# Kernel optimization log

Hardware: AMD Instinct MI355X
Metric: run time of the kernel (lower is better)

The kernel has to match this reference:

```python
import jax, jax.numpy as jnp
import numpy as np

B, L, D, H, DEPTH = 64, 384, 128, 8, 6
DH = D // H          # 16
VOCAB = 32000
C_OUT = 128
FF = 4 * D           # reformer_pytorch default ff_mult=4
SELF_VAL = -5e4      # TOKEN_SELF_ATTN_VALUE
MASK_VAL = -1e9      # causal mask value


def layer_norm(x, g, b, eps=1e-5):
    mu = jnp.mean(x, -1, keepdims=True)
    var = jnp.mean((x - mu) ** 2, -1, keepdims=True)
    return (x - mu) * jax.lax.rsqrt(var + eps) * g + b


def attn_block(x, p):
    # PreNorm + LSHSelfAttention in full-QK-attention fallback (seq <= full_attn_thres)
    h = layer_norm(x, p['ln1_g'], p['ln1_b'])
    qk = (h @ p['Wqk']).reshape(B, L, H, DH).transpose(0, 2, 1, 3)  # [B,H,L,DH]
    v = (h @ p['Wv']).reshape(B, L, H, DH).transpose(0, 2, 1, 3)
    # shared QK: q = qk, k = l2-normalized qk
    k = qk / jnp.maximum(jnp.linalg.norm(qk, axis=-1, keepdims=True), 1e-12)
    dots = jnp.einsum('bhid,bhjd->bhij', qk, k) * (DH ** -0.5)
    i = jnp.arange(L)
    eye = i[:, None] == i[None, :]
    future = i[None, :] > i[:, None]
    dots = jnp.where(eye, SELF_VAL, dots)   # token cannot (easily) attend to itself
    dots = jnp.where(future, MASK_VAL, dots)  # causal
    a = jax.nn.softmax(dots, axis=-1)
    o = jnp.einsum('bhij,bhjd->bhid', a, v).transpose(0, 2, 1, 3).reshape(B, L, D)
    return o @ p['Wo'] + p['bo']


def ff_block(x, p):
    h = layer_norm(x, p['ln2_g'], p['ln2_b'])
    h = jax.nn.gelu(h @ p['W1'] + p['b1'], approximate=False)
    return h @ p['W2'] + p['b2']


def forward(x_enc, emb, pos1, pos2, ln1_g, ln1_b, Wqk, Wv, Wo, bo,
            ln2_g, ln2_b, W1, b1, W2, b2, lnf_g, lnf_b, Wp, bp):
    # axial positional embedding (summed mode): (25,D) + (25,D) -> (625,D)
    pos = (pos1[:, None, :] + pos2[None, :, :]).reshape(25 * 25, D)[:L]
    x = emb[x_enc] + pos  # [B,L,D]

    layer_params = dict(ln1_g=ln1_g, ln1_b=ln1_b, Wqk=Wqk, Wv=Wv, Wo=Wo, bo=bo,
                        ln2_g=ln2_g, ln2_b=ln2_b, W1=W1, b1=b1, W2=W2, b2=b2)

    def block(carry, p):
        x1, x2 = carry
        y1 = x1 + attn_block(x2, p)
        y2 = x2 + ff_block(y1, p)
        return (y1, y2), None

    # reversible-net math: duplicate stream, run blocks, average the two halves
    (x1, x2), _ = jax.lax.scan(block, (x, x), layer_params)
    x = layer_norm((x1 + x2) * 0.5, lnf_g, lnf_b)
    return x.reshape(B, L * D) @ Wp + bp  # [B, C_OUT]


def setup_inputs() -> dict:
    key = jax.random.key(0)
    ks = jax.random.split(key, 12)
    s = 0.02
    inp = {
        'x_enc': jax.random.randint(ks[0], (B, L), 0, VOCAB, dtype=jnp.int32),
        'emb': jax.random.normal(ks[1], (VOCAB, D), jnp.float32) * s,
        'pos1': jax.random.normal(ks[2], (25, D), jnp.float32) * s,
        'pos2': jax.random.normal(ks[3], (25, D), jnp.float32) * s,
        'ln1_g': jnp.ones((DEPTH, D), jnp.float32),
        'ln1_b': jnp.zeros((DEPTH, D), jnp.float32),
        'Wqk': jax.random.normal(ks[4], (DEPTH, D, D), jnp.float32) * s,
        'Wv': jax.random.normal(ks[5], (DEPTH, D, D), jnp.float32) * s,
        'Wo': jax.random.normal(ks[6], (DEPTH, D, D), jnp.float32) * s,
        'bo': jnp.zeros((DEPTH, D), jnp.float32),
        'ln2_g': jnp.ones((DEPTH, D), jnp.float32),
        'ln2_b': jnp.zeros((DEPTH, D), jnp.float32),
        'W1': jax.random.normal(ks[7], (DEPTH, D, FF), jnp.float32) * s,
        'b1': jnp.zeros((DEPTH, FF), jnp.float32),
        'W2': jax.random.normal(ks[8], (DEPTH, FF, D), jnp.float32) * s,
        'b2': jnp.zeros((DEPTH, D), jnp.float32),
        'lnf_g': jnp.ones((D,), jnp.float32),
        'lnf_b': jnp.zeros((D,), jnp.float32),
        'Wp': jax.random.normal(ks[9], (L * D, C_OUT), jnp.float32) * s,
        'bp': jnp.zeros((C_OUT,), jnp.float32),
    }
    return inp


def reference(x_enc, emb, pos1, pos2, ln1_g, ln1_b, Wqk, Wv, Wo, bo,
              ln2_g, ln2_b, W1, b1, W2, b2, lnf_g, lnf_b, Wp, bp):
    return forward(x_enc, emb, pos1, pos2, ln1_g, ln1_b, Wqk, Wv, Wo, bo,
                   ln2_g, ln2_b, W1, b1, W2, b2, lnf_g, lnf_b, Wp, bp)
```

## Files before the change

kernel.cpp:

```cpp
#include <hip/hip_runtime.h>
#include <hip/hip_bf16.h>
#include <math.h>

#define BB 64
#define LL 384
#define DD 128
#define HH 8
#define DHH 16
#define DEPTH 6
#define FFD 512
#define MROWS (BB*LL)
#define COUT 128
#define KP (LL*DD)
#define KSPLIT 96
#define KCHUNK 512

typedef short bf16x8 __attribute__((ext_vector_type(8)));
typedef float f32x4 __attribute__((ext_vector_type(4)));

__device__ __forceinline__ unsigned short f2bs(float x) {
    __hip_bfloat16 h = __float2bfloat16(x);
    return *reinterpret_cast<unsigned short*>(&h);
}
__device__ __forceinline__ float bs2f(unsigned short u) {
    unsigned int v = ((unsigned int)u) << 16;
    return __uint_as_float(v);
}
__device__ __forceinline__ float gelu_exact(float x) {
    return 0.5f * x * (1.0f + erff(x * 0.70710678118654752f));
}

__global__ __launch_bounds__(256) void embedln_kernel(
    const int* __restrict__ x_enc, const float* __restrict__ emb,
    const float* __restrict__ pos1, const float* __restrict__ pos2,
    const float* __restrict__ g, const float* __restrict__ b,
    float* __restrict__ x1, float* __restrict__ x2,
    __hip_bfloat16* __restrict__ y)
{
    int wave = threadIdx.x >> 6;
    int lane = threadIdx.x & 63;
    int row = blockIdx.x * 4 + wave;
    int l = row % LL;
    int tok = x_enc[row];
    float2 e  = ((const float2*)(emb + (size_t)tok * DD))[lane];
    float2 p1 = ((const float2*)(pos1 + (l / 25) * DD))[lane];
    float2 p2 = ((const float2*)(pos2 + (l % 25) * DD))[lane];
    float2 v = make_float2(e.x + p1.x + p2.x, e.y + p1.y + p2.y);
    ((float2*)(x1 + (size_t)row * DD))[lane] = v;
    ((float2*)(x2 + (size_t)row * DD))[lane] = v;
    float2 gg = ((const float2*)g)[lane];
    float2 bb = ((const float2*)b)[lane];
    float s = v.x + v.y;
    float sq = v.x * v.x + v.y * v.y;
    #pragma unroll
    for (int off = 32; off > 0; off >>= 1) {
        s += __shfl_down(s, off, 64);
        sq += __shfl_down(sq, off, 64);
    }
    s = __shfl(s, 0, 64);
    sq = __shfl(sq, 0, 64);
    float mean = s * (1.0f / DD);
    float var = sq * (1.0f / DD) - mean * mean;
    float rstd = rsqrtf(var + 1e-5f);
    __hip_bfloat16* yp = y + (size_t)row * DD + lane * 2;
    yp[0] = __float2bfloat16((v.x - mean) * rstd * gg.x + bb.x);
    yp[1] = __float2bfloat16((v.y - mean) * rstd * gg.y + bb.y);
}

__device__ __forceinline__ void castT_body(
    const float* __restrict__ s, __hip_bfloat16* __restrict__ d,
    int K, int N, int kb, int nb)
{
    __shared__ float tile[32][33];
    int tx = threadIdx.x & 31, ty = threadIdx.x >> 5;
    #pragma unroll
    for (int r = 0; r < 32; r += 8)
        tile[r + ty][tx] = s[(size_t)(kb + r + ty) * N + nb + tx];
    __syncthreads();
    #pragma unroll
    for (int r = 0; r < 32; r += 8)
        d[(size_t)(nb + r + ty) * K + kb + tx] = __float2bfloat16(tile[tx][r + ty]);
}

__global__ __launch_bounds__(256) void cast_all_kernel(
    const float* __restrict__ Wqk, const float* __restrict__ Wv,
    const float* __restrict__ Wo,  const float* __restrict__ W1,
    const float* __restrict__ W2,
    __hip_bfloat16* __restrict__ dqk, __hip_bfloat16* __restrict__ dv,
    __hip_bfloat16* __restrict__ dwo, __hip_bfloat16* __restrict__ d1,
    __hip_bfloat16* __restrict__ d2)
{
    int z = blockIdx.x;
    if (z < 288) {
        int m = z >> 4, t = z & 15;
        int which = m / 6, dd = m % 6;
        const float* s = (which == 0 ? Wqk : (which == 1 ? Wv : Wo)) + (size_t)dd * 16384;
        __hip_bfloat16* d = (which == 0 ? dqk : (which == 1 ? dv : dwo))
                            + (size_t)dd * (which == 2 ? 16384 : 32768);
        castT_body(s, d, 128, 128, (t >> 2) * 32, (t & 3) * 32);
    } else if (z < 672) {
        int i = z - 288; int dd = i >> 6; int t = i & 63;
        castT_body(W1 + (size_t)dd * 65536, d1 + (size_t)dd * 65536,
                   128, 512, (t >> 4) * 32, (t & 15) * 32);
    } else {
        int i = z - 672; int dd = i >> 6; int t = i & 63;
        castT_body(W2 + (size_t)dd * 65536, d2 + (size_t)dd * 65536,
                   512, 128, (t >> 2) * 32, (t & 3) * 32);
    }
}

__global__ __launch_bounds__(256) void castWp_kernel(
    const float* __restrict__ src, __hip_bfloat16* __restrict__ dst)
{
    castT_body(src, dst, KP, 128, blockIdx.x * 32, blockIdx.y * 32);
}

template<int K, int N>
__global__ __launch_bounds__(256) void gemm_qkv_kernel(
    const __hip_bfloat16* __restrict__ A, const __hip_bfloat16* __restrict__ Bt,
    __hip_bfloat16* __restrict__ Cdst)
{
    __shared__ unsigned short As[64 * 128];
    __shared__ unsigned short Bs[128 * 128];
    int tid = threadIdx.x;
    int l = tid & 63, w = tid >> 6;
    int wr = w >> 1, wc = w & 1;
    int lr = l & 15, q = l >> 4;
    int m0 = blockIdx.y * 64;
    int n0 = blockIdx.x * 128;

    f32x4 acc[2][4];
    #pragma unroll
    for (int mt = 0; mt < 2; ++mt)
        #pragma unroll
        for (int nt = 0; nt < 4; ++nt) acc[mt][nt] = (f32x4){0.f, 0.f, 0.f, 0.f};

    for (int kt = 0; kt < K; kt += 128) {
        if (kt) __syncthreads();
        #pragma unroll
        for (int p = 0; p < 4; ++p) {
            int n = p * 256 + tid;
            int r = n >> 4;
            int c = (n & 15) ^ (r & 7);
            *(uint4*)&As[n * 8] = *(const uint4*)(A + (size_t)(m0 + r) * K + kt + c * 8);
        }
        #pragma unroll
        for (int p = 0; p < 8; ++p) {
            int n = p * 256 + tid;
            int r = n >> 4;
            int c = (n & 15) ^ (r & 7);
            *(uint4*)&Bs[n * 8] = *(const uint4*)(Bt + (size_t)(n0 + r) * K + kt + c * 8);
        }
        __syncthreads();
        #pragma unroll
        for (int kk = 0; kk < 4; ++kk) {
            bf16x8 afr[2], bfr[4];
            #pragma unroll
            for (int mt = 0; mt < 2; ++mt) {
                int rA = wr * 32 + mt * 16 + lr;
                int cc = (kk * 4 + q) ^ (rA & 7);
                afr[mt] = *(const bf16x8*)&As[(rA * 16 + cc) * 8];
            }
            #pragma unroll
            for (int nt = 0; nt < 4; ++nt) {
                int rB = wc * 64 + nt * 16 + lr;
                int cc = (kk * 4 + q) ^ (rB & 7);
                bfr[nt] = *(const bf16x8*)&Bs[(rB * 16 + cc) * 8];
            }
            #pragma unroll
            for (int mt = 0; mt < 2; ++mt)
                #pragma unroll
                for (int nt = 0; nt < 4; ++nt)
                    acc[mt][nt] = __builtin_amdgcn_mfma_f32_16x16x32_bf16(
                        afr[mt], bfr[nt], acc[mt][nt], 0, 0, 0);
        }
    }

    #pragma unroll
    for (int mt = 0; mt < 2; ++mt)
        #pragma unroll
        for (int nt = 0; nt < 4; ++nt) {
            int col = n0 + wc * 64 + nt * 16 + lr;
            #pragma unroll
            for (int r = 0; r < 4; ++r) {
                int row = m0 + wr * 32 + mt * 16 + q * 4 + r;
                Cdst[(size_t)row * N + col] = __float2bfloat16(acc[mt][nt][r]);
            }
        }
}

__global__ __launch_bounds__(256) void attn_kernel(
    const __hip_bfloat16* __restrict__ qkv, __hip_bfloat16* __restrict__ o)
{
    int z  = blockIdx.x >> 9;
    int bh = blockIdx.x & 511;
    int b = bh >> 3, hh = bh & 7;
    const unsigned short* base = (const unsigned short*)qkv + (size_t)b * LL * 256 + hh * DHH;

    __shared__ unsigned short knb[LL + 2][24];
    __shared__ unsigned short vtb[16][LL + 24];
    __shared__ float cq[LL];
    __shared__ unsigned short ptile[4][16][40];

    int t = threadIdx.x;
    for (int r = t; r < LL; r += 256) {
        const unsigned short* qp = base + (size_t)r * 256;
        unsigned short qs[16], vs16[16];
        *(uint4*)&qs[0]  = *(const uint4*)(qp);
        *(uint4*)&qs[8]  = *(const uint4*)(qp + 8);
        *(uint4*)&vs16[0] = *(const uint4*)(qp + 128);
        *(uint4*)&vs16[8] = *(const uint4*)(qp + 136);
        float q[16];
        #pragma unroll
        for (int d = 0; d < 16; ++d) q[d] = bs2f(qs[d]);
        float nrm = 0.f;
        #pragma unroll
        for (int d = 0; d < 16; ++d) nrm = fmaf(q[d], q[d], nrm);
        float qn = sqrtf(nrm);
        float inv = 1.0f / fmaxf(qn, 1e-12f);
        cq[r] = 0.25f * qn;
        unsigned short kb[16];
        #pragma unroll
        for (int d = 0; d < 16; ++d) kb[d] = f2bs(q[d] * inv);
        *(uint4*)&knb[r][0] = *(uint4*)&kb[0];
        *(uint4*)&knb[r][8] = *(uint4*)&kb[8];
        *(uint4*)&knb[r][16] = make_uint4(0u, 0u, 0u, 0u);
        #pragma unroll
        for (int d = 0; d < 16; ++d) vtb[d][r] = vs16[d];
    }
    if (t < 16) {
        #pragma unroll
        for (int c = 0; c < 24; ++c) vtb[t][LL + c] = 0;
    }
    if (t < 2) {
        #pragma unroll
        for (int c = 0; c < 24; ++c) knb[LL + t][c] = 0;
    }

    int w = t >> 6, l = t & 63;
    int lr = l & 15, q4 = l >> 4;
    __syncthreads();

    bf16x8 zfrag = {0, 0, 0, 0, 0, 0, 0, 0};
    bf16x8 onesf;
    #pragma unroll
    for (int i = 0; i < 8; ++i) onesf[i] = (short)0x3F80;

    int slot = 2 * w + z;
    int strips[3] = { slot, 15 - slot, 16 + slot };
    #pragma unroll
    for (int si = 0; si < 3; ++si) {
        int s = strips[si];
        int r0 = s * 16;
        bf16x8 bq = *(const bf16x8*)&knb[r0 + lr][q4 * 8];
        float ccq = cq[r0 + lr];
        int qg = r0 + lr;

        f32x4 oacc = (f32x4){0.f, 0.f, 0.f, 0.f};
        f32x4 lacc = (f32x4){0.f, 0.f, 0.f, 0.f};

        for (int jt = 0; jt <= s; jt += 2) {
            bf16x8 a0 = *(const bf16x8*)&knb[jt * 16 + lr][(q4 & 1) * 8];
            a0 = (q4 < 2) ? a0 : zfrag;
            bf16x8 a1 = *(const bf16x8*)&knb[(jt + 1) * 16 + lr][(q4 & 1) * 8];
            a1 = (q4 < 2) ? a1 : zfrag;
            f32x4 s0 = __builtin_amdgcn_mfma_f32_16x16x32_bf16(
                a0, bq, (f32x4){0.f, 0.f, 0.f, 0.f}, 0, 0, 0);
            f32x4 s1 = __builtin_amdgcn_mfma_f32_16x16x32_bf16(
                a1, bq, (f32x4){0.f, 0.f, 0.f, 0.f}, 0, 0, 0);

            unsigned int pk0[2], pk1[2];
            #pragma unroll
            for (int h = 0; h < 2; ++h) {
                int ja = jt * 16 + q4 * 4 + 2 * h;
                float pa = __expf(fmaf(s0[2 * h],     ccq, -ccq));
                pa = (ja < qg) ? pa : 0.f;
                float pb = __expf(fmaf(s0[2 * h + 1], ccq, -ccq));
                pb = (ja + 1 < qg) ? pb : 0.f;
                pk0[h] = (unsigned int)f2bs(pa) | ((unsigned int)f2bs(pb) << 16);
                float pc = __expf(fmaf(s1[2 * h],     ccq, -ccq));
                pc = (ja + 16 < qg) ? pc : 0.f;
                float pd = __expf(fmaf(s1[2 * h + 1], ccq, -ccq));
                pd = (ja + 17 < qg) ? pd : 0.f;
                pk1[h] = (unsigned int)f2bs(pc) | ((unsigned int)f2bs(pd) << 16);
            }
            *(uint2*)&ptile[w][lr][q4 * 4]      = make_uint2(pk0[0], pk0[1]);
            *(uint2*)&ptile[w][lr][16 + q4 * 4] = make_uint2(pk1[0], pk1[1]);
            asm volatile("s_waitcnt lgkmcnt(0)" ::: "memory");
            bf16x8 pfrag = *(const bf16x8*)&ptile[w][lr][q4 * 8];
            bf16x8 vfrag = *(const bf16x8*)&vtb[lr][jt * 16 + q4 * 8];
            oacc = __builtin_amdgcn_mfma_f32_16x16x32_bf16(pfrag, vfrag, oacc, 0, 0, 0);
            lacc = __builtin_amdgcn_mfma_f32_16x16x32_bf16(pfrag, onesf, lacc, 0, 0, 0);
        }

        if (s == 0 && q4 == 0) {
            lacc[0] = 1.0f;
            oacc[0] = bs2f(vtb[lr][0]);
        }
        unsigned short* ob = (unsigned short*)o + (size_t)(b * LL + r0) * DD + hh * 16 + lr;
        #pragma unroll
        for (int reg = 0; reg < 4; ++reg) {
            float ov = oacc[reg] / lacc[reg];
            ob[(size_t)(q4 * 4 + reg) * DD] = f2bs(ov);
        }
    }
}

__global__ __launch_bounds__(256) void mega_wolf_kernel(
    const __hip_bfloat16* __restrict__ Ao, const __hip_bfloat16* __restrict__ WoTd,
    const float* __restrict__ bod, float* __restrict__ x1,
    const float* __restrict__ lng, const float* __restrict__ lnb,
    const __hip_bfloat16* __restrict__ W1Td, const float* __restrict__ b1d,
    __hip_bfloat16* __restrict__ hff)
{
    __shared__ unsigned short As[64 * 128];
    __shared__ unsigned short Bs[128 * 128];
    __shared__ unsigned short Hs[64 * 128];
    int tid = threadIdx.x;
    int l = tid & 63, w = tid >> 6;
    int wr = w >> 1, wc = w & 1;
    int lr = l & 15, q = l >> 4;
    int m0 = blockIdx.x * 64;

    f32x4 acc[2][4];
    #pragma unroll
    for (int mt = 0; mt < 2; ++mt)
        #pragma unroll
        for (int nt = 0; nt < 4; ++nt) acc[mt][nt] = (f32x4){0.f, 0.f, 0.f, 0.f};

    #pragma unroll
    for (int p = 0; p < 4; ++p) {
        int n = p * 256 + tid;
        int r = n >> 4;
        int c = (n & 15) ^ (r & 7);
        *(uint4*)&As[n * 8] = *(const uint4*)(Ao + (size_t)(m0 + r) * 128 + c * 8);
    }
    #pragma unroll
    for (int p = 0; p < 8; ++p) {
        int n = p * 256 + tid;
        int r = n >> 4;
        int c = (n & 15) ^ (r & 7);
        *(uint4*)&Bs[n * 8] = *(const uint4*)(WoTd + (size_t)r * 128 + c * 8);
    }
    __syncthreads();
    #pragma unroll
    for (int kk = 0; kk < 4; ++kk) {
        bf16x8 afr[2], bfr[4];
        #pragma unroll
        for (int mt = 0; mt < 2; ++mt) {
            int rA = wr * 32 + mt * 16 + lr;
            int cc = (kk * 4 + q) ^ (rA & 7);
            afr[mt] = *(const bf16x8*)&As[(rA * 16 + cc) * 8];
        }
        #pragma unroll
        for (int nt = 0; nt < 4; ++nt) {
            int rB = wc * 64 + nt * 16 + lr;
            int cc = (kk * 4 + q) ^ (rB & 7);
            bfr[nt] = *(const bf16x8*)&Bs[(rB * 16 + cc) * 8];
        }
        #pragma unroll
        for (int mt = 0; mt < 2; ++mt)
            #pragma unroll
            for (int nt = 0; nt < 4; ++nt)
                acc[mt][nt] = __builtin_amdgcn_mfma_f32_16x16x32_bf16(
                    afr[mt], bfr[nt], acc[mt][nt], 0, 0, 0);
    }

    float* fp = (float*)Bs;
    __syncthreads();
    #pragma unroll
    for (int mt = 0; mt < 2; ++mt)
        #pragma unroll
        for (int nt = 0; nt < 4; ++nt) {
            int col = wc * 64 + nt * 16 + lr;
            float bv = bod[col];
            #pragma unroll
            for (int r = 0; r < 4; ++r) {
                int rowL = wr * 32 + mt * 16 + q * 4 + r;
                fp[rowL * 128 + col] = acc[mt][nt][r] + bv
                                       + x1[(size_t)(m0 + rowL) * 128 + col];
            }
        }
    __syncthreads();
    {
        int rl = tid >> 2, sub = tid & 3;
        float s = 0.f, sq = 0.f;
        #pragma unroll
        for (int c4 = 0; c4 < 8; ++c4) {
            float4 v = *(const float4*)&fp[rl * 128 + sub * 32 + c4 * 4];
            s  += (v.x + v.y) + (v.z + v.w);
            sq += (v.x * v.x + v.y * v.y) + (v.z * v.z + v.w * v.w);
        }
        s  += __shfl_xor(s, 1);  s  += __shfl_xor(s, 2);
        sq += __shfl_xor(sq, 1); sq += __shfl_xor(sq, 2);
        float mean = s * (1.0f / 128.0f);
        float var  = sq * (1.0f / 128.0f) - mean * mean;
        float rstd = rsqrtf(var + 1e-5f);
        #pragma unroll
        for (int c4 = 0; c4 < 8; ++c4) {
            int col = sub * 32 + c4 * 4;
            float4 v  = *(const float4*)&fp[rl * 128 + col];
            *(float4*)(x1 + (size_t)(m0 + rl) * 128 + col) = v;
            float4 g4 = *(const float4*)(lng + col);
            float4 b4 = *(const float4*)(lnb + col);
            unsigned short pk[4];
            pk[0] = f2bs((v.x - mean) * rstd * g4.x + b4.x);
            pk[1] = f2bs((v.y - mean) * rstd * g4.y + b4.y);
            pk[2] = f2bs((v.z - mean) * rstd * g4.z + b4.z);
            pk[3] = f2bs((v.w - mean) * rstd * g4.w + b4.w);
            int addr = rl * 128 + (((col >> 3) ^ (rl & 7)) << 3) + (col & 7);
            *(ushort4*)&Hs[addr] = *(ushort4*)&pk[0];
        }
    }
    __syncthreads();

    for (int nc = 0; nc < 4; ++nc) {
        if (nc) __syncthreads();
        #pragma unroll
        for (int p = 0; p < 8; ++p) {
            int n = p * 256 + tid;
            int r = n >> 4;
            int c = (n & 15) ^ (r & 7);
            *(uint4*)&Bs[n * 8] = *(const uint4*)(W1Td + (size_t)(nc * 128 + r) * 128 + c * 8);
        }
        __syncthreads();
        f32x4 a2[2][4];
        #pragma unroll
        for (int mt = 0; mt < 2; ++mt)
            #pragma unroll
            for (int nt = 0; nt < 4; ++nt) a2[mt][nt] = (f32x4){0.f, 0.f, 0.f, 0.f};
        #pragma unroll
        for (int kk = 0; kk < 4; ++kk) {
            bf16x8 afr[2], bfr[4];
            #pragma unroll
            for (int mt = 0; mt < 2; ++mt) {
                int rA = wr * 32 + mt * 16 + lr;
                int cc = (kk * 4 + q) ^ (rA & 7);
                afr[mt] = *(const bf16x8*)&Hs[(rA * 16 + cc) * 8];
            }
            #pragma unroll
            for (int nt = 0; nt < 4; ++nt) {
                int rB = wc * 64 + nt * 16 + lr;
                int cc = (kk * 4 + q) ^ (rB & 7);
                bfr[nt] = *(const bf16x8*)&Bs[(rB * 16 + cc) * 8];
            }
            #pragma unroll
            for (int mt = 0; mt < 2; ++mt)
                #pragma unroll
                for (int nt = 0; nt < 4; ++nt)
                    a2[mt][nt] = __builtin_amdgcn_mfma_f32_16x16x32_bf16(
                        afr[mt], bfr[nt], a2[mt][nt], 0, 0, 0);
        }
        #pragma unroll
        for (int mt = 0; mt < 2; ++mt)
            #pragma unroll
            for (int nt = 0; nt < 4; ++nt) {
                int colg = nc * 128 + wc * 64 + nt * 16 + lr;
                float bv = b1d[colg];
                #pragma unroll
                for (int r = 0; r < 4; ++r) {
                    int row = m0 + wr * 32 + mt * 16 + q * 4 + r;
                    hff[(size_t)row * 512 + colg] =
                        __float2bfloat16(gelu_exact(a2[mt][nt][r] + bv));
                }
            }
    }
}

template<bool LAST>
__global__ __launch_bounds__(256) void mega_ffq_kernel(
    const __hip_bfloat16* __restrict__ Ahff, const __hip_bfloat16* __restrict__ W2Td,
    const float* __restrict__ b2d, float* __restrict__ x2,
    const float* __restrict__ x1,
    const float* __restrict__ lng, const float* __restrict__ lnb,
    const __hip_bfloat16* __restrict__ WqvTd, __hip_bfloat16* __restrict__ qkv,
    __hip_bfloat16* __restrict__ hout)
{
    __shared__ unsigned short As[64 * 128];
    __shared__ unsigned short Bs[128 * 128];
    __shared__ unsigned short Hs[64 * 128];
    int tid = threadIdx.x;
    int l = tid & 63, w = tid >> 6;
    int wr = w >> 1, wc = w & 1;
    int lr = l & 15, q = l >> 4;
    int m0 = blockIdx.x * 64;

    f32x4 acc[2][4];
    #pragma unroll
    for (int mt = 0; mt < 2; ++mt)
        #pragma unroll
        for (int nt = 0; nt < 4; ++nt) acc[mt][nt] = (f32x4){0.f, 0.f, 0.f, 0.f};

    for (int kt = 0; kt < 512; kt += 128) {
        if (kt) __syncthreads();
        #pragma unroll
        for (int p = 0; p < 4; ++p) {
            int n = p * 256 + tid;
            int r = n >> 4;
            int c = (n & 15) ^ (r & 7);
            *(uint4*)&As[n * 8] = *(const uint4*)(Ahff + (size_t)(m0 + r) * 512 + kt + c * 8);
        }
        #pragma unroll
        for (int p = 0; p < 8; ++p) {
            int n = p * 256 + tid;
            int r = n >> 4;
            int c = (n & 15) ^ (r & 7);
            *(uint4*)&Bs[n * 8] = *(const uint4*)(W2Td + (size_t)r * 512 + kt + c * 8);
        }
        __syncthreads();
        #pragma unroll
        for (int kk = 0; kk < 4; ++kk) {
            bf16x8 afr[2], bfr[4];
            #pragma unroll
            for (int mt = 0; mt < 2; ++mt) {
                int rA = wr * 32 + mt * 16 + lr;
                int cc = (kk * 4 + q) ^ (rA & 7);
                afr[mt] = *(const bf16x8*)&As[(rA * 16 + cc) * 8];
            }
            #pragma unroll
            for (int nt = 0; nt < 4; ++nt) {
                int rB = wc * 64 + nt * 16 + lr;
                int cc = (kk * 4 + q) ^ (rB & 7);
                bfr[nt] = *(const bf16x8*)&Bs[(rB * 16 + cc) * 8];
            }
            #pragma unroll
            for (int mt = 0; mt < 2; ++mt)
                #pragma unroll
                for (int nt = 0; nt < 4; ++nt)
                    acc[mt][nt] = __builtin_amdgcn_mfma_f32_16x16x32_bf16(
                        afr[mt], bfr[nt], acc[mt][nt], 0, 0, 0);
        }
    }

    float* fp = (float*)Bs;
    __syncthreads();
    #pragma unroll
    for (int mt = 0; mt < 2; ++mt)
        #pragma unroll
        for (int nt = 0; nt < 4; ++nt) {
            int col = wc * 64 + nt * 16 + lr;
            float bv = b2d[col];
            #pragma unroll
            for (int r = 0; r < 4; ++r) {
                int rowL = wr * 32 + mt * 16 + q * 4 + r;
                fp[rowL * 128 + col] = acc[mt][nt][r] + bv
                                       + x2[(size_t)(m0 + rowL) * 128 + col];
            }
        }
    __syncthreads();
    {
        int rl = tid >> 2, sub = tid & 3;
        float s = 0.f, sq = 0.f;
        #pragma unroll
        for (int c4 = 0; c4 < 8; ++c4) {
            float4 v = *(const float4*)&fp[rl * 128 + sub * 32 + c4 * 4];
            if (LAST) {
                float4 xo = *(const float4*)(x1 + (size_t)(m0 + rl) * 128 + sub * 32 + c4 * 4);
                v.x = (v.x + xo.x) * 0.5f; v.y = (v.y + xo.y) * 0.5f;
                v.z = (v.z + xo.z) * 0.5f; v.w = (v.w + xo.w) * 0.5f;
            }
            s  += (v.x + v.y) + (v.z + v.w);
            sq += (v.x * v.x + v.y * v.y) + (v.z * v.z + v.w * v.w);
        }
        s  += __shfl_xor(s, 1);  s  += __shfl_xor(s, 2);
        sq += __shfl_xor(sq, 1); sq += __shfl_xor(sq, 2);
        float mean = s * (1.0f / 128.0f);
        float var  = sq * (1.0f / 128.0f) - mean * mean;
        float rstd = rsqrtf(var + 1e-5f);
        #pragma unroll
        for (int c4 = 0; c4 < 8; ++c4) {
            int col = sub * 32 + c4 * 4;
            float4 v = *(const float4*)&fp[rl * 128 + col];
            if (LAST) {
                float4 xo = *(const float4*)(x1 + (size_t)(m0 + rl) * 128 + col);
                v.x = (v.x + xo.x) * 0.5f; v.y = (v.y + xo.y) * 0.5f;
                v.z = (v.z + xo.z) * 0.5f; v.w = (v.w + xo.w) * 0.5f;
            } else {
                *(float4*)(x2 + (size_t)(m0 + rl) * 128 + col) = v;
            }
            float4 g4 = *(const float4*)(lng + col);
            float4 b4 = *(const float4*)(lnb + col);
            unsigned short pk[4];
            pk[0] = f2bs((v.x - mean) * rstd * g4.x + b4.x);
            pk[1] = f2bs((v.y - mean) * rstd * g4.y + b4.y);
            pk[2] = f2bs((v.z - mean) * rstd * g4.z + b4.z);
            pk[3] = f2bs((v.w - mean) * rstd * g4.w + b4.w);
            if (LAST) {
                *(ushort4*)((unsigned short*)hout + (size_t)(m0 + rl) * 128 + col)
                    = *(ushort4*)&pk[0];
            } else {
                int addr = rl * 128 + (((col >> 3) ^ (rl & 7)) << 3) + (col & 7);
                *(ushort4*)&Hs[addr] = *(ushort4*)&pk[0];
            }
        }
    }
    __syncthreads();

    if (!LAST) {
        for (int nc = 0; nc < 2; ++nc) {
            if (nc) __syncthreads();
            #pragma unroll
            for (int p = 0; p < 8; ++p) {
                int n = p * 256 + tid;
                int r = n >> 4;
                int c = (n & 15) ^ (r & 7);
                *(uint4*)&Bs[n * 8] = *(const uint4*)(WqvTd + (size_t)(nc * 128 + r) * 128 + c * 8);
            }
            __syncthreads();
            f32x4 a2[2][4];
            #pragma unroll
            for (int mt = 0; mt < 2; ++mt)
                #pragma unroll
                for (int nt = 0; nt < 4; ++nt) a2[mt][nt] = (f32x4){0.f, 0.f, 0.f, 0.f};
            #pragma unroll
            for (int kk = 0; kk < 4; ++kk) {
                bf16x8 afr[2], bfr[4];
                #pragma unroll
                for (int mt = 0; mt < 2; ++mt) {
                    int rA = wr * 32 + mt * 16 + lr;
                    int cc = (kk * 4 + q) ^ (rA & 7);
                    afr[mt] = *(const bf16x8*)&Hs[(rA * 16 + cc) * 8];
                }
                #pragma unroll
                for (int nt = 0; nt < 4; ++nt) {
                    int rB = wc * 64 + nt * 16 + lr;
                    int cc = (kk * 4 + q) ^ (rB & 7);
                    bfr[nt] = *(const bf16x8*)&Bs[(rB * 16 + cc) * 8];
                }
                #pragma unroll
                for (int mt = 0; mt < 2; ++mt)
                    #pragma unroll
                    for (int nt = 0; nt < 4; ++nt)
                        a2[mt][nt] = __builtin_amdgcn_mfma_f32_16x16x32_bf16(
                            afr[mt], bfr[nt], a2[mt][nt], 0, 0, 0);
            }
            #pragma unroll
            for (int mt = 0; mt < 2; ++mt)
                #pragma unroll
                for (int nt = 0; nt < 4; ++nt) {
                    int colg = nc * 128 + wc * 64 + nt * 16 + lr;
                    #pragma unroll
                    for (int r = 0; r < 4; ++r) {
                        int row = m0 + wr * 32 + mt * 16 + q * 4 + r;
                        qkv[(size_t)row * 256 + colg] = __float2bfloat16(a2[mt][nt][r]);
                    }
                }
        }
    }
}

__global__ __launch_bounds__(256) void final_mfma_kernel(
    const __hip_bfloat16* __restrict__ A, const __hip_bfloat16* __restrict__ Bt,
    float* __restrict__ partials)
{
    __shared__ unsigned short As[64 * 128];
    __shared__ unsigned short Bs[128 * 128];
    int tid = threadIdx.x;
    int l = tid & 63, w = tid >> 6;
    int wr = w >> 1, wc = w & 1;
    int lr = l & 15, q = l >> 4;
    int kbase = blockIdx.x * KCHUNK;

    f32x4 acc[2][4];
    #pragma unroll
    for (int mt = 0; mt < 2; ++mt)
        #pragma unroll
        for (int nt = 0; nt < 4; ++nt) acc[mt][nt] = (f32x4){0.f, 0.f, 0.f, 0.f};

    for (int kt = 0; kt < KCHUNK; kt += 128) {
        if (kt) __syncthreads();
        #pragma unroll
        for (int p = 0; p < 4; ++p) {
            int n = p * 256 + tid;
            int r = n >> 4;
            int c = (n & 15) ^ (r & 7);
            *(uint4*)&As[n * 8] = *(const uint4*)(A + (size_t)r * KP + kbase + kt + c * 8);
        }
        #pragma unroll
        for (int p = 0; p < 8; ++p) {
            int n = p * 256 + tid;
            int r = n >> 4;
            int c = (n & 15) ^ (r & 7);
            *(uint4*)&Bs[n * 8] = *(const uint4*)(Bt + (size_t)r * KP + kbase + kt + c * 8);
        }
        __syncthreads();
        #pragma unroll
        for (int kk = 0; kk < 4; ++kk) {
            bf16x8 afr[2], bfr[4];
            #pragma unroll
            for (int mt = 0; mt < 2; ++mt) {
                int rA = wr * 32 + mt * 16 + lr;
                int cc = (kk * 4 + q) ^ (rA & 7);
                afr[mt] = *(const bf16x8*)&As[(rA * 16 + cc) * 8];
            }
            #pragma unroll
            for (int nt = 0; nt < 4; ++nt) {
                int rB = wc * 64 + nt * 16 + lr;
                int cc = (kk * 4 + q) ^ (rB & 7);
                bfr[nt] = *(const bf16x8*)&Bs[(rB * 16 + cc) * 8];
            }
            #pragma unroll
            for (int mt = 0; mt < 2; ++mt)
                #pragma unroll
                for (int nt = 0; nt < 4; ++nt)
                    acc[mt][nt] = __builtin_amdgcn_mfma_f32_16x16x32_bf16(
                        afr[mt], bfr[nt], acc[mt][nt], 0, 0, 0);
        }
    }

    float* dst = partials + (size_t)blockIdx.x * (64 * 128);
    #pragma unroll
    for (int mt = 0; mt < 2; ++mt)
        #pragma unroll
        for (int nt = 0; nt < 4; ++nt) {
            int col = wc * 64 + nt * 16 + lr;
            #pragma unroll
            for (int r = 0; r < 4; ++r) {
                int row = wr * 32 + mt * 16 + q * 4 + r;
                dst[row * 128 + col] = acc[mt][nt][r];
            }
        }
}

__global__ __launch_bounds__(256) void final_reduce_kernel(
    const float* __restrict__ partials, const float* __restrict__ bp,
    float* __restrict__ out)
{
    int j = blockIdx.x * 256 + threadIdx.x;
    float s = bp[j & (COUT - 1)];
    #pragma unroll 8
    for (int p = 0; p < KSPLIT; ++p)
        s += partials[(size_t)p * 8192 + j];
    out[j] = s;
}

extern "C" void kernel_launch(void* const* d_in, const int* in_sizes, int n_in,
                              void* d_out, int out_size, void* d_ws, size_t ws_size,
                              hipStream_t stream)
{
    const int*   x_enc = (const int*)  d_in[0];
    const float* emb   = (const float*)d_in[1];
    const float* pos1  = (const float*)d_in[2];
    const float* pos2  = (const float*)d_in[3];
    const float* ln1_g = (const float*)d_in[4];
    const float* ln1_b = (const float*)d_in[5];
    const float* Wqk   = (const float*)d_in[6];
    const float* Wv    = (const float*)d_in[7];
    const float* Wo    = (const float*)d_in[8];
    const float* bo    = (const float*)d_in[9];
    const float* ln2_g = (const float*)d_in[10];
    const float* ln2_b = (const float*)d_in[11];
    const float* W1    = (const float*)d_in[12];
    const float* b1    = (const float*)d_in[13];
    const float* W2    = (const float*)d_in[14];
    const float* b2    = (const float*)d_in[15];
    const float* lnf_g = (const float*)d_in[16];
    const float* lnf_b = (const float*)d_in[17];
    const float* Wp    = (const float*)d_in[18];
    const float* bp    = (const float*)d_in[19];
    float* out = (float*)d_out;

    const size_t SZ = (size_t)MROWS * DD;
    float* ws_f = (float*)d_ws;
    float* x1 = ws_f;
    float* x2 = ws_f + SZ;
    __hip_bfloat16* hff  = (__hip_bfloat16*)(ws_f + 2 * SZ);
    __hip_bfloat16* h_bf = (__hip_bfloat16*)(ws_f + 4 * SZ);
    __hip_bfloat16* o_bf = h_bf + SZ;
    __hip_bfloat16* wqvT = o_bf + SZ;
    __hip_bfloat16* woT  = wqvT + 6 * 32768;
    __hip_bfloat16* w1T  = woT  + 6 * 16384;
    __hip_bfloat16* w2T  = w1T  + 6 * 65536;
    __hip_bfloat16* WpT  = w2T  + 6 * 65536;
    __hip_bfloat16* qkv  = WpT;
    float* partials = (float*)(WpT + (size_t)COUT * KP);

    cast_all_kernel<<<dim3(1056), dim3(256), 0, stream>>>(
        Wqk, Wv, Wo, W1, W2, wqvT, wqvT + 16384, woT, w1T, w2T);
    embedln_kernel<<<dim3(MROWS / 4), dim3(256), 0, stream>>>(
        x_enc, emb, pos1, pos2, ln1_g, ln1_b, x1, x2, h_bf);
    gemm_qkv_kernel<128, 256><<<dim3(2, MROWS / 64), dim3(256), 0, stream>>>(
        h_bf, wqvT, qkv);

    for (int d = 0; d < DEPTH; ++d) {
        attn_kernel<<<dim3(BB * HH * 2), dim3(256), 0, stream>>>(qkv, o_bf);
        mega_wolf_kernel<<<dim3(MROWS / 64), dim3(256), 0, stream>>>(
            o_bf, woT + (size_t)d * 16384, bo + d * DD, x1,
            ln2_g + d * DD, ln2_b + d * DD,
            w1T + (size_t)d * 65536, b1 + d * FFD, hff);
        if (d < DEPTH - 1) {
            mega_ffq_kernel<false><<<dim3(MROWS / 64), dim3(256), 0, stream>>>(
                hff, w2T + (size_t)d * 65536, b2 + d * DD, x2, nullptr,
                ln1_g + (d + 1) * DD, ln1_b + (d + 1) * DD,
                wqvT + (size_t)(d + 1) * 32768, qkv, nullptr);
        } else {
            mega_ffq_kernel<true><<<dim3(MROWS / 64), dim3(256), 0, stream>>>(
                hff, w2T + (size_t)d * 65536, b2 + d * DD, x2, x1,
                lnf_g, lnf_b, nullptr, nullptr, h_bf);
        }
    }

    castWp_kernel<<<dim3(KP / 32, 4), dim3(256), 0, stream>>>(Wp, WpT);
    final_mfma_kernel<<<dim3(KSPLIT), dim3(256), 0, stream>>>(h_bf, WpT, partials);
    final_reduce_kernel<<<dim3(32), dim3(256), 0, stream>>>(partials, bp, out);
}
```

Measured before the change: 619.2 us.

## Fuse Wo/FF1 and FF2/QKV kernels into one per-layer kernel

Merges the Wo+LN2+FF1 kernel and the FF2+LN1+QKV kernel into a single per-layer kernel. The GELU output of each 128-column FF1 chunk goes into shared memory and is consumed at once as a K-chunk of the FF2 GEMM, so the 64x512 bf16 hidden activation never round-trips through global memory. This removes one launch per layer and the hff buffer traffic. The cost is more serialized work per block and extra barriers, and possibly higher register use from the persistent FF2 accumulators, which may lower occupancy.

```diff
diff --git a/kernel.cpp b/kernel.cpp
--- a/kernel.cpp
+++ b/kernel.cpp
@@ -306,12 +306,17 @@
     }
 }
 
-__global__ __launch_bounds__(256) void mega_wolf_kernel(
+template<bool LAST>
+__global__ __launch_bounds__(256) void mega_layer_kernel(
     const __hip_bfloat16* __restrict__ Ao, const __hip_bfloat16* __restrict__ WoTd,
     const float* __restrict__ bod, float* __restrict__ x1,
-    const float* __restrict__ lng, const float* __restrict__ lnb,
+    const float* __restrict__ ln2g, const float* __restrict__ ln2b,
     const __hip_bfloat16* __restrict__ W1Td, const float* __restrict__ b1d,
-    __hip_bfloat16* __restrict__ hff)
+    const __hip_bfloat16* __restrict__ W2Td, const float* __restrict__ b2d,
+    float* __restrict__ x2,
+    const float* __restrict__ ln1g, const float* __restrict__ ln1b,
+    const __hip_bfloat16* __restrict__ WqvTd, __hip_bfloat16* __restrict__ qkv,
+    __hip_bfloat16* __restrict__ hout)
 {
     __shared__ unsigned short As[64 * 128];
     __shared__ unsigned short Bs[128 * 128];
@@ -401,8 +406,8 @@
             int col = sub * 32 + c4 * 4;
             float4 v  = *(const float4*)&fp[rl * 128 + col];
             *(float4*)(x1 + (size_t)(m0 + rl) * 128 + col) = v;
-            float4 g4 = *(const float4*)(lng + col);
-            float4 b4 = *(const float4*)(lnb + col);
+            float4 g4 = *(const float4*)(ln2g + col);
+            float4 b4 = *(const float4*)(ln2b + col);
             unsigned short pk[4];
             pk[0] = f2bs((v.x - mean) * rstd * g4.x + b4.x);
             pk[1] = f2bs((v.y - mean) * rstd * g4.y + b4.y);
@@ -414,6 +419,12 @@
     }
     __syncthreads();
 
+    f32x4 ffacc[2][4];
+    #pragma unroll
+    for (int mt = 0; mt < 2; ++mt)
+        #pragma unroll
+        for (int nt = 0; nt < 4; ++nt) ffacc[mt][nt] = (f32x4){0.f, 0.f, 0.f, 0.f};
+
     for (int nc = 0; nc < 4; ++nc) {
         if (nc) __syncthreads();
         #pragma unroll
@@ -424,11 +435,11 @@
             *(uint4*)&Bs[n * 8] = *(const uint4*)(W1Td + (size_t)(nc * 128 + r) * 128 + c * 8);
         }
         __syncthreads();
-        f32x4 a2[2][4];
+        f32x4 a1[2][4];
         #pragma unroll
         for (int mt = 0; mt < 2; ++mt)
             #pragma unroll
-            for (int nt = 0; nt < 4; ++nt) a2[mt][nt] = (f32x4){0.f, 0.f, 0.f, 0.f};
+            for (int nt = 0; nt < 4; ++nt) a1[mt][nt] = (f32x4){0.f, 0.f, 0.f, 0.f};
         #pragma unroll
         for (int kk = 0; kk < 4; ++kk) {
             bf16x8 afr[2], bfr[4];
@@ -448,64 +459,29 @@
             for (int mt = 0; mt < 2; ++mt)
                 #pragma unroll
                 for (int nt = 0; nt < 4; ++nt)
-                    a2[mt][nt] = __builtin_amdgcn_mfma_f32_16x16x32_bf16(
-                        afr[mt], bfr[nt], a2[mt][nt], 0, 0, 0);
+                    a1[mt][nt] = __builtin_amdgcn_mfma_f32_16x16x32_bf16(
+                        afr[mt], bfr[nt], a1[mt][nt], 0, 0, 0);
         }
         #pragma unroll
         for (int mt = 0; mt < 2; ++mt)
             #pragma unroll
             for (int nt = 0; nt < 4; ++nt) {
-                int colg = nc * 128 + wc * 64 + nt * 16 + lr;
-                float bv = b1d[colg];
+                int k = wc * 64 + nt * 16 + lr;
+                float bv = b1d[nc * 128 + k];
                 #pragma unroll
                 for (int r = 0; r < 4; ++r) {
-                    int row = m0 + wr * 32 + mt * 16 + q * 4 + r;
-                    hff[(size_t)row * 512 + colg] =
-                        __float2bfloat16(gelu_exact(a2[mt][nt][r] + bv));
+                    int row = wr * 32 + mt * 16 + q * 4 + r;
+                    int addr = row * 128 + (((k >> 3) ^ (row & 7)) << 3) + (k & 7);
+                    As[addr] = f2bs(gelu_exact(a1[mt][nt][r] + bv));
                 }
             }
-    }
-}
-
-template<bool LAST>
-__global__ __launch_bounds__(256) void mega_ffq_kernel(
-    const __hip_bfloat16* __restrict__ Ahff, const __hip_bfloat16* __restrict__ W2Td,
-    const float* __restrict__ b2d, float* __restrict__ x2,
-    const float* __restrict__ x1,
-    const float* __restrict__ lng, const float* __restrict__ lnb,
-    const __hip_bfloat16* __restrict__ WqvTd, __hip_bfloat16* __restrict__ qkv,
-    __hip_bfloat16* __restrict__ hout)
-{
-    __shared__ unsigned short As[64 * 128];
-    __shared__ unsigned short Bs[128 * 128];
-    __shared__ unsigned short Hs[64 * 128];
-    int tid = threadIdx.x;
-    int l = tid & 63, w = tid >> 6;
-    int wr = w >> 1, wc = w & 1;
-    int lr = l & 15, q = l >> 4;
-    int m0 = blockIdx.x * 64;
-
-    f32x4 acc[2][4];
-    #pragma unroll
-    for (int mt = 0; mt < 2; ++mt)
-        #pragma unroll
-        for (int nt = 0; nt < 4; ++nt) acc[mt][nt] = (f32x4){0.f, 0.f, 0.f, 0.f};
-
-    for (int kt = 0; kt < 512; kt += 128) {
-        if (kt) __syncthreads();
-        #pragma unroll
-        for (int p = 0; p < 4; ++p) {
-            int n = p * 256 + tid;
-            int r = n >> 4;
-            int c = (n & 15) ^ (r & 7);
-            *(uint4*)&As[n * 8] = *(const uint4*)(Ahff + (size_t)(m0 + r) * 512 + kt + c * 8);
-        }
+        __syncthreads();
         #pragma unroll
         for (int p = 0; p < 8; ++p) {
             int n = p * 256 + tid;
             int r = n >> 4;
             int c = (n & 15) ^ (r & 7);
-            *(uint4*)&Bs[n * 8] = *(const uint4*)(W2Td + (size_t)r * 512 + kt + c * 8);
+            *(uint4*)&Bs[n * 8] = *(const uint4*)(W2Td + (size_t)r * 512 + nc * 128 + c * 8);
         }
         __syncthreads();
         #pragma unroll
@@ -527,12 +503,11 @@
             for (int mt = 0; mt < 2; ++mt)
                 #pragma unroll
                 for (int nt = 0; nt < 4; ++nt)
-                    acc[mt][nt] = __builtin_amdgcn_mfma_f32_16x16x32_bf16(
-                        afr[mt], bfr[nt], acc[mt][nt], 0, 0, 0);
-        }
-    }
-
-    float* fp = (float*)Bs;
+                    ffacc[mt][nt] = __builtin_amdgcn_mfma_f32_16x16x32_bf16(
+                        afr[mt], bfr[nt], ffacc[mt][nt], 0, 0, 0);
+        }
+    }
+
     __syncthreads();
     #pragma unroll
     for (int mt = 0; mt < 2; ++mt)
@@ -543,7 +518,7 @@
             #pragma unroll
             for (int r = 0; r < 4; ++r) {
                 int rowL = wr * 32 + mt * 16 + q * 4 + r;
-                fp[rowL * 128 + col] = acc[mt][nt][r] + bv
+                fp[rowL * 128 + col] = ffacc[mt][nt][r] + bv
                                        + x2[(size_t)(m0 + rowL) * 128 + col];
             }
         }
@@ -578,8 +553,8 @@
             } else {
                 *(float4*)(x2 + (size_t)(m0 + rl) * 128 + col) = v;
             }
-            float4 g4 = *(const float4*)(lng + col);
-            float4 b4 = *(const float4*)(lnb + col);
+            float4 g4 = *(const float4*)(ln1g + col);
+            float4 b4 = *(const float4*)(ln1b + col);
             unsigned short pk[4];
             pk[0] = f2bs((v.x - mean) * rstd * g4.x + b4.x);
             pk[1] = f2bs((v.y - mean) * rstd * g4.y + b4.y);
@@ -764,8 +739,7 @@
     float* ws_f = (float*)d_ws;
     float* x1 = ws_f;
     float* x2 = ws_f + SZ;
-    __hip_bfloat16* hff  = (__hip_bfloat16*)(ws_f + 2 * SZ);
-    __hip_bfloat16* h_bf = (__hip_bfloat16*)(ws_f + 4 * SZ);
+    __hip_bfloat16* h_bf = (__hip_bfloat16*)(ws_f + 2 * SZ);
     __hip_bfloat16* o_bf = h_bf + SZ;
     __hip_bfloat16* wqvT = o_bf + SZ;
     __hip_bfloat16* woT  = wqvT + 6 * 32768;
@@ -784,18 +758,20 @@
 
     for (int d = 0; d < DEPTH; ++d) {
         attn_kernel<<<dim3(BB * HH * 2), dim3(256), 0, stream>>>(qkv, o_bf);
-        mega_wolf_kernel<<<dim3(MROWS / 64), dim3(256), 0, stream>>>(
-            o_bf, woT + (size_t)d * 16384, bo + d * DD, x1,
-            ln2_g + d * DD, ln2_b + d * DD,
-            w1T + (size_t)d * 65536, b1 + d * FFD, hff);
         if (d < DEPTH - 1) {
-            mega_ffq_kernel<false><<<dim3(MROWS / 64), dim3(256), 0, stream>>>(
-                hff, w2T + (size_t)d * 65536, b2 + d * DD, x2, nullptr,
+            mega_layer_kernel<false><<<dim3(MROWS / 64), dim3(256), 0, stream>>>(
+                o_bf, woT + (size_t)d * 16384, bo + d * DD, x1,
+                ln2_g + d * DD, ln2_b + d * DD,
+                w1T + (size_t)d * 65536, b1 + d * FFD,
+                w2T + (size_t)d * 65536, b2 + d * DD, x2,
                 ln1_g + (d + 1) * DD, ln1_b + (d + 1) * DD,
                 wqvT + (size_t)(d + 1) * 32768, qkv, nullptr);
         } else {
-            mega_ffq_kernel<true><<<dim3(MROWS / 64), dim3(256), 0, stream>>>(
-                hff, w2T + (size_t)d * 65536, b2 + d * DD, x2, x1,
+            mega_layer_kernel<true><<<dim3(MROWS / 64), dim3(256), 0, stream>>>(
+                o_bf, woT + (size_t)d * 16384, bo + d * DD, x1,
+                ln2_g + d * DD, ln2_b + d * DD,
+                w1T + (size_t)d * 65536, b1 + d * FFD,
+                w2T + (size_t)d * 65536, b2 + d * DD, x2,
                 lnf_g, lnf_b, nullptr, nullptr, h_bf);
         }
     }
```

Result: slower. 712.1 us (+15.0%).
